# Kernel optimization log

Measured on AMD Instinct MI355X. Metric: run time of the kernel, lower is better.

## Reference

```python
import jax, jax.numpy as jnp
import numpy as np

# Dims: B=batch, T=attention source length, V=vector_size, A=attention_length (A==V forced by broadcast).
# TF Conv2D(kernel=(1,V), padding=SAME) on a [B,T,1,C] input has spatial width 1, so only the
# kernel column at pad_before=(V-1)//2 touches real data -> equivalent to a per-timestep matmul.
# We therefore materialize just that effective column (Wk_enc: [V,A], Kc_cov: [A] for the
# 1-channel coverage conv). Math is identical to the original layer.

def setup_inputs() -> dict:
    key = jax.random.key(0)
    ks = jax.random.split(key, 8)
    B, T, V = 32, 8192, 128
    A = V
    return {
        "encoder_state": jax.random.normal(ks[0], (B, T, V), jnp.float32),
        "decoder_state": jax.random.normal(ks[1], (B, V), jnp.float32),
        "input_mask": jnp.ones((B, T), jnp.float32),
        "coverage": jax.random.uniform(ks[2], (B, T, 1, 1), jnp.float32),
        "Wk_enc": jax.random.normal(ks[3], (V, A), jnp.float32) * 0.05,  # effective encoder conv column
        "b_enc": jnp.zeros((A,), jnp.float32),
        "W_dec": jax.random.normal(ks[4], (V, A), jnp.float32) * 0.05,  # Dense(vector_size)
        "b_dec": jnp.zeros((A,), jnp.float32),
        "Kc_cov": jax.random.normal(ks[5], (A,), jnp.float32) * 0.05,   # effective coverage conv column (1 in-channel)
        "b_cov": jnp.zeros((A,), jnp.float32),
        "v": jax.random.normal(ks[6], (A,), jnp.float32),
    }


def reference(encoder_state, decoder_state, input_mask, coverage,
              Wk_enc, b_enc, W_dec, b_dec, Kc_cov, b_cov, v):
    # encoder conv features: [B,T,A]
    enc_feat = jnp.einsum('btv,va->bta', encoder_state, Wk_enc) + b_enc
    # decoder dense features: [B,A]
    dec_feat = decoder_state @ W_dec + b_dec
    # coverage conv features: [B,T,A] (coverage has 1 channel, width 1)
    cov = coverage[:, :, 0, 0]                       # [B,T]
    cov_feat = cov[:, :, None] * Kc_cov + b_cov       # [B,T,A]
    # additive score: e[b,t] = sum_a v[a] * tanh(...)
    e = jnp.einsum('bta,a->bt',
                   jnp.tanh(enc_feat + dec_feat[:, None, :] + cov_feat), v)
    # masked softmax with renormalization
    attn = jax.nn.softmax(e, axis=-1) * input_mask
    attn = attn / jnp.sum(attn, axis=-1, keepdims=True)
    # coverage accumulation
    coverage_out = coverage + attn[:, :, None, None]
    # context vector: [B,V]
    context = jnp.einsum('bt,btv->bv', attn, encoder_state)
    return context, attn, coverage_out
```

## Files before the change

### kernel.cpp

```cpp
#include <hip/hip_runtime.h>
#include <hip/hip_bf16.h>
#include <math.h>

typedef __bf16 bf16x8 __attribute__((ext_vector_type(8)));
typedef float  f32x4  __attribute__((ext_vector_type(4)));

#define B_ 32
#define T_ 8192

__device__ __forceinline__ float tanh_fast(float x) {
  float ex = __expf(2.0f * x);
  return 1.0f - 2.0f / (ex + 1.0f);
}

__global__ __launch_bounds__(256) void setup_kernel(
    const float* __restrict__ dec, const float* __restrict__ b_enc,
    const float* __restrict__ W_dec, const float* __restrict__ b_dec,
    const float* __restrict__ b_cov, const float* __restrict__ Wk,
    float* __restrict__ addbuf, __bf16* __restrict__ wfrag)
{
  const int blk = blockIdx.x, tid = threadIdx.x;
  if (blk < 16) {
    const int idx = blk * 256 + tid;
    const int b = idx >> 7, a = idx & 127;
    float acc = b_dec[a] + b_enc[a] + b_cov[a];
    for (int k = 0; k < 128; ++k)
      acc += dec[b * 128 + k] * W_dec[k * 128 + a];
    addbuf[idx] = acc;
  } else {
    const int f = (blk - 16) * 256 + tid;
    const int l = f & 63;
    const int rest = f >> 6;
    const int ks = rest & 3, ct = rest >> 2;
    for (int j = 0; j < 8; ++j) {
      const int k = ks * 32 + (l >> 4) * 8 + j;
      const int a = ct * 16 + (l & 15);
      wfrag[f * 8 + j] = (__bf16)Wk[k * 128 + a];
    }
  }
}

__global__ __launch_bounds__(256, 4) void feat_ctx_kernel(
    const float* __restrict__ enc, const float* __restrict__ cov,
    const float* __restrict__ mask,
    const __bf16* __restrict__ wfrag_g, const float* __restrict__ addbuf,
    const float* __restrict__ Kc, const float* __restrict__ vvec,
    float* __restrict__ p_out, float* __restrict__ pctx,
    float* __restrict__ mblk, float* __restrict__ sblk)
{
  __shared__ __align__(16) float smem[8192];
  const int tid  = threadIdx.x;
  const int lane = tid & 63;
  const int w    = tid >> 6;
  const int lr   = lane & 15;
  const int lg   = lane >> 4;
  const long rowbase = (long)blockIdx.x * 128 + w * 32;
  const int b = (int)(rowbase >> 13);

  {
    const float4* src = (const float4*)wfrag_g;
    float4* dst = (float4*)smem;
#pragma unroll
    for (int i = 0; i < 8; ++i) dst[tid + i * 256] = src[tid + i * 256];
  }

  bf16x8 afrag[2][4];
#pragma unroll
  for (int rt = 0; rt < 2; ++rt) {
    const float* rp = enc + (rowbase + rt * 16 + lr) * 128;
#pragma unroll
    for (int ks = 0; ks < 4; ++ks) {
      const float4 f0 = *(const float4*)(rp + ks * 32 + lg * 8);
      const float4 f1 = *(const float4*)(rp + ks * 32 + lg * 8 + 4);
      bf16x8 t;
      t[0]=(__bf16)f0.x; t[1]=(__bf16)f0.y; t[2]=(__bf16)f0.z; t[3]=(__bf16)f0.w;
      t[4]=(__bf16)f1.x; t[5]=(__bf16)f1.y; t[6]=(__bf16)f1.z; t[7]=(__bf16)f1.w;
      afrag[rt][ks] = t;
    }
  }

  float addc[8], kcc[8], vc[8];
#pragma unroll
  for (int ct = 0; ct < 8; ++ct) {
    const int col = ct * 16 + lr;
    addc[ct] = addbuf[b * 128 + col];
    kcc[ct]  = Kc[col];
    vc[ct]   = vvec[col];
  }
  float cv8[2][4];
#pragma unroll
  for (int rt = 0; rt < 2; ++rt)
#pragma unroll
    for (int q = 0; q < 4; ++q)
      cv8[rt][q] = cov[rowbase + rt * 16 + lg * 4 + q];

  __syncthreads();

  float pacc[2][4];
#pragma unroll
  for (int rt = 0; rt < 2; ++rt)
#pragma unroll
    for (int q = 0; q < 4; ++q) pacc[rt][q] = 0.f;

  const bf16x8* wf = (const bf16x8*)smem;
#pragma unroll
  for (int ct = 0; ct < 8; ++ct) {
    bf16x8 bfr[4];
#pragma unroll
    for (int ks = 0; ks < 4; ++ks) bfr[ks] = wf[(ct * 4 + ks) * 64 + lane];
    f32x4 a0 = {0.f, 0.f, 0.f, 0.f};
    f32x4 a1 = {0.f, 0.f, 0.f, 0.f};
#pragma unroll
    for (int ks = 0; ks < 4; ++ks) {
      a0 = __builtin_amdgcn_mfma_f32_16x16x32_bf16(afrag[0][ks], bfr[ks], a0, 0, 0, 0);
      a1 = __builtin_amdgcn_mfma_f32_16x16x32_bf16(afrag[1][ks], bfr[ks], a1, 0, 0, 0);
    }
#pragma unroll
    for (int q = 0; q < 4; ++q) {
      const float x0 = a0[q] + addc[ct] + cv8[0][q] * kcc[ct];
      const float x1 = a1[q] + addc[ct] + cv8[1][q] * kcc[ct];
      pacc[0][q] += tanh_fast(x0) * vc[ct];
      pacc[1][q] += tanh_fast(x1) * vc[ct];
    }
  }

  float e8[2][4];
#pragma unroll
  for (int rt = 0; rt < 2; ++rt)
#pragma unroll
    for (int q = 0; q < 4; ++q) {
      float p = pacc[rt][q];
      p += __shfl_xor(p, 1); p += __shfl_xor(p, 2);
      p += __shfl_xor(p, 4); p += __shfl_xor(p, 8);
      e8[rt][q] = p;
    }

  float wm = e8[0][0];
#pragma unroll
  for (int rt = 0; rt < 2; ++rt)
#pragma unroll
    for (int q = 0; q < 4; ++q) wm = fmaxf(wm, e8[rt][q]);
  wm = fmaxf(wm, __shfl_xor(wm, 16));
  wm = fmaxf(wm, __shfl_xor(wm, 32));

  __syncthreads();
  float* red = smem;
  if (lane == 0) red[w] = wm;
  __syncthreads();
  const float m_loc = fmaxf(fmaxf(red[0], red[1]), fmaxf(red[2], red[3]));

  float p8[2][4];
  float ps = 0.f;
#pragma unroll
  for (int rt = 0; rt < 2; ++rt)
#pragma unroll
    for (int q = 0; q < 4; ++q) {
      const float mk = mask[rowbase + rt * 16 + lg * 4 + q];
      const float pv = __expf(e8[rt][q] - m_loc) * mk;
      p8[rt][q] = pv; ps += pv;
    }
#pragma unroll
  for (int off = 32; off > 0; off >>= 1) ps += __shfl_xor(ps, off);
  if (lane == 0) red[4 + w] = ps;
  __syncthreads();
  if (tid == 0) {
    sblk[blockIdx.x] = (red[4] + red[5] + red[6] + red[7]) * (1.0f / 16.0f);
    mblk[blockIdx.x] = m_loc;
  }

  float prow[2];
#pragma unroll
  for (int rt = 0; rt < 2; ++rt) {
    const int r3 = lr & 3;
    float sel = p8[rt][0];
    sel = (r3 == 1) ? p8[rt][1] : sel;
    sel = (r3 == 2) ? p8[rt][2] : sel;
    sel = (r3 == 3) ? p8[rt][3] : sel;
    prow[rt] = __shfl(sel, ((lr >> 2) << 4) | lr);
  }
  if (lg < 2) p_out[rowbase + lg * 16 + lr] = (lg == 0) ? prow[0] : prow[1];

  float ctxp[32];
#pragma unroll
  for (int c = 0; c < 32; ++c) ctxp[c] = 0.f;
#pragma unroll
  for (int rt = 0; rt < 2; ++rt) {
    const float pr = prow[rt];
#pragma unroll
    for (int ks = 0; ks < 4; ++ks)
#pragma unroll
      for (int j = 0; j < 8; ++j)
        ctxp[ks * 8 + j] += pr * (float)afrag[rt][ks][j];
  }
#pragma unroll
  for (int m = 1; m <= 8; m <<= 1)
#pragma unroll
    for (int c = 0; c < 32; ++c) ctxp[c] += __shfl_xor(ctxp[c], m);

  float* ctx_lds = smem + 8;
  if (lr == 0) {
#pragma unroll
    for (int ks = 0; ks < 4; ++ks)
#pragma unroll
      for (int j = 0; j < 8; ++j)
        ctx_lds[w * 128 + ks * 32 + lg * 8 + j] = ctxp[ks * 8 + j];
  }
  __syncthreads();
  if (tid < 128) {
    const float s = ctx_lds[tid] + ctx_lds[128 + tid] +
                    ctx_lds[256 + tid] + ctx_lds[384 + tid];
    pctx[(long)blockIdx.x * 128 + tid] = s;
  }
}

__global__ __launch_bounds__(128) void reduce_kernel(
    const float* __restrict__ mblk, const float* __restrict__ sblk,
    const float* __restrict__ pctx, float* __restrict__ alpha,
    float* __restrict__ ctx)
{
  const int b = blockIdx.x, tid = threadIdx.x;
  __shared__ float al[64];
  if (tid < 64) {
    const float mi = mblk[b * 64 + tid];
    const float si = sblk[b * 64 + tid];
    float m = mi;
#pragma unroll
    for (int off = 32; off > 0; off >>= 1) m = fmaxf(m, __shfl_xor(m, off));
    const float a = __expf(mi - m);
    float z = si * a;
#pragma unroll
    for (int off = 32; off > 0; off >>= 1) z += __shfl_xor(z, off);
    const float ai = a / z;
    al[tid] = ai;
    alpha[b * 64 + tid] = ai;
  }
  __syncthreads();
  float acc = 0.f;
#pragma unroll 8
  for (int i = 0; i < 64; ++i)
    acc += pctx[(long)(b * 64 + i) * 128 + tid] * al[i];
  ctx[b * 128 + tid] = acc;
}

__global__ __launch_bounds__(256) void finish_kernel(
    const float* __restrict__ p_buf, const float* __restrict__ alpha,
    const float* __restrict__ cov, float* __restrict__ attn,
    float* __restrict__ covout)
{
  const long idx = (long)blockIdx.x * 256 + threadIdx.x;
  const float a = p_buf[idx] * alpha[idx >> 7];
  attn[idx] = a;
  covout[idx] = cov[idx] + a;
}

extern "C" void kernel_launch(void* const* d_in, const int* in_sizes, int n_in,
                              void* d_out, int out_size, void* d_ws, size_t ws_size,
                              hipStream_t stream) {
  const float* enc   = (const float*)d_in[0];
  const float* dec   = (const float*)d_in[1];
  const float* mask  = (const float*)d_in[2];
  const float* cov   = (const float*)d_in[3];
  const float* Wk    = (const float*)d_in[4];
  const float* b_enc = (const float*)d_in[5];
  const float* W_dec = (const float*)d_in[6];
  const float* b_dec = (const float*)d_in[7];
  const float* Kc    = (const float*)d_in[8];
  const float* b_cov = (const float*)d_in[9];
  const float* vvec  = (const float*)d_in[10];

  float* out    = (float*)d_out;
  float* ctx    = out;
  float* attn   = out + B_ * 128;
  float* covout = attn + B_ * T_;

  char* ws = (char*)d_ws;
  __bf16* wfrag  = (__bf16*)ws;
  float*  addbuf = (float*)(ws + 32768);
  float*  p_buf  = (float*)(ws + 49152);
  float*  pctx   = (float*)(ws + 49152 + 1048576);
  float*  mblk   = (float*)(ws + 49152 + 2097152);
  float*  sblk   = (float*)(ws + 49152 + 2105344);
  float*  alpha  = (float*)(ws + 49152 + 2113536);

  setup_kernel   <<<24,   256, 0, stream>>>(dec, b_enc, W_dec, b_dec, b_cov, Wk,
                                            addbuf, wfrag);
  feat_ctx_kernel<<<2048, 256, 0, stream>>>(enc, cov, mask, wfrag, addbuf, Kc, vvec,
                                            p_buf, pctx, mblk, sblk);
  reduce_kernel  <<<32,   128, 0, stream>>>(mblk, sblk, pctx, alpha, ctx);
  finish_kernel  <<<1024, 256, 0, stream>>>(p_buf, alpha, cov, attn, covout);
}
```

Before: 57.06 us.

## Use transpose-style butterfly reductions and parallelize context reduce across more threads

Replaces the redundant xor-shuffle reductions of scores and context partials with recursive-halving butterflies, where each lane keeps half the values at every step. This cuts the shuffle count, especially for the 32-wide context vector. It also vectorizes the coverage load, drops one block barrier by moving the sblk/mblk writes to the end, and splits the per-batch reduce kernel over 1024 threads with an LDS combine. The risk is in the lane-to-row index mapping, which is more intricate and easy to get wrong.

```diff
diff --git a/kernel.cpp b/kernel.cpp
--- a/kernel.cpp
+++ b/kernel.cpp
@@ -87,12 +87,9 @@
     kcc[ct]  = Kc[col];
     vc[ct]   = vvec[col];
   }
-  float cv8[2][4];
-#pragma unroll
-  for (int rt = 0; rt < 2; ++rt)
-#pragma unroll
-    for (int q = 0; q < 4; ++q)
-      cv8[rt][q] = cov[rowbase + rt * 16 + lg * 4 + q];
+  const float4 cvA = *(const float4*)(cov + rowbase + lg * 4);
+  const float4 cvB = *(const float4*)(cov + rowbase + 16 + lg * 4);
+  float cv8[2][4] = {{cvA.x, cvA.y, cvA.z, cvA.w}, {cvB.x, cvB.y, cvB.z, cvB.w}};
 
   __syncthreads();
 
@@ -124,22 +121,34 @@
     }
   }
 
-  float e8[2][4];
-#pragma unroll
-  for (int rt = 0; rt < 2; ++rt)
-#pragma unroll
-    for (int q = 0; q < 4; ++q) {
-      float p = pacc[rt][q];
-      p += __shfl_xor(p, 1); p += __shfl_xor(p, 2);
-      p += __shfl_xor(p, 4); p += __shfl_xor(p, 8);
-      e8[rt][q] = p;
-    }
-
-  float wm = e8[0][0];
-#pragma unroll
-  for (int rt = 0; rt < 2; ++rt)
-#pragma unroll
-    for (int q = 0; q < 4; ++q) wm = fmaxf(wm, e8[rt][q]);
+  const bool b0 = (lr & 1), b1 = ((lr >> 1) & 1), b2 = ((lr >> 2) & 1);
+  float e4[4];
+#pragma unroll
+  for (int m = 0; m < 4; ++m) {
+    const float keep = b0 ? pacc[1][m] : pacc[0][m];
+    const float send = b0 ? pacc[0][m] : pacc[1][m];
+    e4[m] = keep + __shfl_xor(send, 1);
+  }
+  float e2[2];
+#pragma unroll
+  for (int m = 0; m < 2; ++m) {
+    const float keep = b1 ? e4[2 + m] : e4[m];
+    const float send = b1 ? e4[m] : e4[2 + m];
+    e2[m] = keep + __shfl_xor(send, 2);
+  }
+  float eo;
+  {
+    const float keep = b2 ? e2[1] : e2[0];
+    const float send = b2 ? e2[0] : e2[1];
+    eo = keep + __shfl_xor(send, 4);
+  }
+  eo += __shfl_xor(eo, 8);
+  const int row_own = (lr & 1) * 16 + lg * 4 + ((lr >> 1) & 1) * 2 + ((lr >> 2) & 1);
+
+  float wm = eo;
+  wm = fmaxf(wm, __shfl_xor(wm, 1));
+  wm = fmaxf(wm, __shfl_xor(wm, 2));
+  wm = fmaxf(wm, __shfl_xor(wm, 4));
   wm = fmaxf(wm, __shfl_xor(wm, 16));
   wm = fmaxf(wm, __shfl_xor(wm, 32));
 
@@ -149,34 +158,21 @@
   __syncthreads();
   const float m_loc = fmaxf(fmaxf(red[0], red[1]), fmaxf(red[2], red[3]));
 
-  float p8[2][4];
-  float ps = 0.f;
-#pragma unroll
-  for (int rt = 0; rt < 2; ++rt)
-#pragma unroll
-    for (int q = 0; q < 4; ++q) {
-      const float mk = mask[rowbase + rt * 16 + lg * 4 + q];
-      const float pv = __expf(e8[rt][q] - m_loc) * mk;
-      p8[rt][q] = pv; ps += pv;
-    }
-#pragma unroll
-  for (int off = 32; off > 0; off >>= 1) ps += __shfl_xor(ps, off);
+  const float p_own = __expf(eo - m_loc) * mask[rowbase + row_own];
+  float ps = p_own;
+  ps += __shfl_xor(ps, 1);
+  ps += __shfl_xor(ps, 2);
+  ps += __shfl_xor(ps, 4);
+  ps += __shfl_xor(ps, 16);
+  ps += __shfl_xor(ps, 32);
   if (lane == 0) red[4 + w] = ps;
-  __syncthreads();
-  if (tid == 0) {
-    sblk[blockIdx.x] = (red[4] + red[5] + red[6] + red[7]) * (1.0f / 16.0f);
-    mblk[blockIdx.x] = m_loc;
-  }
 
   float prow[2];
 #pragma unroll
   for (int rt = 0; rt < 2; ++rt) {
-    const int r3 = lr & 3;
-    float sel = p8[rt][0];
-    sel = (r3 == 1) ? p8[rt][1] : sel;
-    sel = (r3 == 2) ? p8[rt][2] : sel;
-    sel = (r3 == 3) ? p8[rt][3] : sel;
-    prow[rt] = __shfl(sel, ((lr >> 2) << 4) | lr);
+    const int q = lr & 3;
+    const int src = rt + ((q >> 1) << 1) + ((q & 1) << 2) + ((lr >> 2) << 4);
+    prow[rt] = __shfl(p_own, src);
   }
   if (lg < 2) p_out[rowbase + lg * 16 + lr] = (lg == 0) ? prow[0] : prow[1];
 
@@ -192,18 +188,42 @@
       for (int j = 0; j < 8; ++j)
         ctxp[ks * 8 + j] += pr * (float)afrag[rt][ks][j];
   }
-#pragma unroll
-  for (int m = 1; m <= 8; m <<= 1)
-#pragma unroll
-    for (int c = 0; c < 32; ++c) ctxp[c] += __shfl_xor(ctxp[c], m);
-
-  float* ctx_lds = smem + 8;
-  if (lr == 0) {
-#pragma unroll
-    for (int ks = 0; ks < 4; ++ks)
-#pragma unroll
-      for (int j = 0; j < 8; ++j)
-        ctx_lds[w * 128 + ks * 32 + lg * 8 + j] = ctxp[ks * 8 + j];
+
+  const bool b3 = ((lr >> 3) & 1);
+  float v16[16];
+#pragma unroll
+  for (int m = 0; m < 16; ++m) {
+    const float keep = b0 ? ctxp[2 * m + 1] : ctxp[2 * m];
+    const float send = b0 ? ctxp[2 * m] : ctxp[2 * m + 1];
+    v16[m] = keep + __shfl_xor(send, 1);
+  }
+  float v8[8];
+#pragma unroll
+  for (int m = 0; m < 8; ++m) {
+    const float keep = b1 ? v16[2 * m + 1] : v16[2 * m];
+    const float send = b1 ? v16[2 * m] : v16[2 * m + 1];
+    v8[m] = keep + __shfl_xor(send, 2);
+  }
+  float v4[4];
+#pragma unroll
+  for (int m = 0; m < 4; ++m) {
+    const float keep = b2 ? v8[2 * m + 1] : v8[2 * m];
+    const float send = b2 ? v8[2 * m] : v8[2 * m + 1];
+    v4[m] = keep + __shfl_xor(send, 4);
+  }
+  float v2[2];
+#pragma unroll
+  for (int m = 0; m < 2; ++m) {
+    const float keep = b3 ? v4[2 * m + 1] : v4[2 * m];
+    const float send = b3 ? v4[2 * m] : v4[2 * m + 1];
+    v2[m] = keep + __shfl_xor(send, 8);
+  }
+  float* ctx_lds = smem + 16;
+#pragma unroll
+  for (int m = 0; m < 2; ++m) {
+    const int c = 16 * m + lr;
+    const int v = (c >> 3) * 32 + lg * 8 + (c & 7);
+    ctx_lds[w * 128 + v] = v2[m];
   }
   __syncthreads();
   if (tid < 128) {
@@ -211,15 +231,20 @@
                     ctx_lds[256 + tid] + ctx_lds[384 + tid];
     pctx[(long)blockIdx.x * 128 + tid] = s;
   }
-}
-
-__global__ __launch_bounds__(128) void reduce_kernel(
+  if (tid == 0) {
+    sblk[blockIdx.x] = red[4] + red[5] + red[6] + red[7];
+    mblk[blockIdx.x] = m_loc;
+  }
+}
+
+__global__ __launch_bounds__(1024) void reduce_kernel(
     const float* __restrict__ mblk, const float* __restrict__ sblk,
     const float* __restrict__ pctx, float* __restrict__ alpha,
     float* __restrict__ ctx)
 {
   const int b = blockIdx.x, tid = threadIdx.x;
   __shared__ float al[64];
+  __shared__ float part[8][128];
   if (tid < 64) {
     const float mi = mblk[b * 64 + tid];
     const float si = sblk[b * 64 + tid];
@@ -235,11 +260,21 @@
     alpha[b * 64 + tid] = ai;
   }
   __syncthreads();
+  const int v = tid & 127, ch = tid >> 7;
   float acc = 0.f;
-#pragma unroll 8
-  for (int i = 0; i < 64; ++i)
-    acc += pctx[(long)(b * 64 + i) * 128 + tid] * al[i];
-  ctx[b * 128 + tid] = acc;
+#pragma unroll
+  for (int k = 0; k < 8; ++k) {
+    const int i = ch * 8 + k;
+    acc += pctx[(long)(b * 64 + i) * 128 + v] * al[i];
+  }
+  part[ch][v] = acc;
+  __syncthreads();
+  if (tid < 128) {
+    float s = 0.f;
+#pragma unroll
+    for (int c = 0; c < 8; ++c) s += part[c][tid];
+    ctx[b * 128 + tid] = s;
+  }
 }
 
 __global__ __launch_bounds__(256) void finish_kernel(
@@ -286,6 +321,6 @@
                                             addbuf, wfrag);
   feat_ctx_kernel<<<2048, 256, 0, stream>>>(enc, cov, mask, wfrag, addbuf, Kc, vvec,
                                             p_buf, pctx, mblk, sblk);
-  reduce_kernel  <<<32,   128, 0, stream>>>(mblk, sblk, pctx, alpha, ctx);
+  reduce_kernel  <<<32,  1024, 0, stream>>>(mblk, sblk, pctx, alpha, ctx);
   finish_kernel  <<<1024, 256, 0, stream>>>(p_buf, alpha, cov, attn, covout);
 }
```

After: 72.78 us. +27.5%, slower.

## Split context computation into a second fp32 pass over encoder state

Applied to the files above, without the earlier changes.

The feature kernel no longer computes partial context vectors. It now computes softmax statistics per wavefront instead of per block, which drops the block-level LDS reductions and barriers. A new alpha kernel turns the 256 per-chunk max/sum pairs into rescale factors. A fused ctx_attn kernel then rescales the probabilities, writes attn and coverage, and recomputes the context by re-reading the full fp32 encoder tensor, accumulating with atomicAdd. This aims to cut register pressure and synchronisation in the main kernel, but it reads the 128 MB encoder tensor a second time. Context is now computed in full fp32 rather than from bf16-converted values.

```diff
diff --git a/kernel.cpp b/kernel.cpp
--- a/kernel.cpp
+++ b/kernel.cpp
@@ -40,13 +40,13 @@
   }
 }
 
-__global__ __launch_bounds__(256, 4) void feat_ctx_kernel(
+__global__ __launch_bounds__(256, 4) void feat_kernel(
     const float* __restrict__ enc, const float* __restrict__ cov,
     const float* __restrict__ mask,
     const __bf16* __restrict__ wfrag_g, const float* __restrict__ addbuf,
     const float* __restrict__ Kc, const float* __restrict__ vvec,
-    float* __restrict__ p_out, float* __restrict__ pctx,
-    float* __restrict__ mblk, float* __restrict__ sblk)
+    float* __restrict__ p_out, float* __restrict__ mchunk,
+    float* __restrict__ schunk)
 {
   __shared__ __align__(16) float smem[8192];
   const int tid  = threadIdx.x;
@@ -54,7 +54,8 @@
   const int w    = tid >> 6;
   const int lr   = lane & 15;
   const int lg   = lane >> 4;
-  const long rowbase = (long)blockIdx.x * 128 + w * 32;
+  const int chunk = blockIdx.x * 4 + w;
+  const long rowbase = (long)chunk * 32;
   const int b = (int)(rowbase >> 13);
 
   {
@@ -79,20 +80,9 @@
     }
   }
 
-  float addc[8], kcc[8], vc[8];
-#pragma unroll
-  for (int ct = 0; ct < 8; ++ct) {
-    const int col = ct * 16 + lr;
-    addc[ct] = addbuf[b * 128 + col];
-    kcc[ct]  = Kc[col];
-    vc[ct]   = vvec[col];
-  }
-  float cv8[2][4];
-#pragma unroll
-  for (int rt = 0; rt < 2; ++rt)
-#pragma unroll
-    for (int q = 0; q < 4; ++q)
-      cv8[rt][q] = cov[rowbase + rt * 16 + lg * 4 + q];
+  const float4 cvA = *(const float4*)(cov + rowbase + lg * 4);
+  const float4 cvB = *(const float4*)(cov + rowbase + 16 + lg * 4);
+  float cv8[2][4] = {{cvA.x, cvA.y, cvA.z, cvA.w}, {cvB.x, cvB.y, cvB.z, cvB.w}};
 
   __syncthreads();
 
@@ -108,6 +98,10 @@
     bf16x8 bfr[4];
 #pragma unroll
     for (int ks = 0; ks < 4; ++ks) bfr[ks] = wf[(ct * 4 + ks) * 64 + lane];
+    const int col = ct * 16 + lr;
+    const float addc = addbuf[b * 128 + col];
+    const float kcc  = Kc[col];
+    const float vc   = vvec[col];
     f32x4 a0 = {0.f, 0.f, 0.f, 0.f};
     f32x4 a1 = {0.f, 0.f, 0.f, 0.f};
 #pragma unroll
@@ -117,10 +111,10 @@
     }
 #pragma unroll
     for (int q = 0; q < 4; ++q) {
-      const float x0 = a0[q] + addc[ct] + cv8[0][q] * kcc[ct];
-      const float x1 = a1[q] + addc[ct] + cv8[1][q] * kcc[ct];
-      pacc[0][q] += tanh_fast(x0) * vc[ct];
-      pacc[1][q] += tanh_fast(x1) * vc[ct];
+      const float x0 = a0[q] + addc + cv8[0][q] * kcc;
+      const float x1 = a1[q] + addc + cv8[1][q] * kcc;
+      pacc[0][q] += tanh_fast(x0) * vc;
+      pacc[1][q] += tanh_fast(x1) * vc;
     }
   }
 
@@ -135,19 +129,13 @@
       e8[rt][q] = p;
     }
 
-  float wm = e8[0][0];
-#pragma unroll
-  for (int rt = 0; rt < 2; ++rt)
-#pragma unroll
-    for (int q = 0; q < 4; ++q) wm = fmaxf(wm, e8[rt][q]);
-  wm = fmaxf(wm, __shfl_xor(wm, 16));
-  wm = fmaxf(wm, __shfl_xor(wm, 32));
-
-  __syncthreads();
-  float* red = smem;
-  if (lane == 0) red[w] = wm;
-  __syncthreads();
-  const float m_loc = fmaxf(fmaxf(red[0], red[1]), fmaxf(red[2], red[3]));
+  float m_loc = e8[0][0];
+#pragma unroll
+  for (int rt = 0; rt < 2; ++rt)
+#pragma unroll
+    for (int q = 0; q < 4; ++q) m_loc = fmaxf(m_loc, e8[rt][q]);
+  m_loc = fmaxf(m_loc, __shfl_xor(m_loc, 16));
+  m_loc = fmaxf(m_loc, __shfl_xor(m_loc, 32));
 
   float p8[2][4];
   float ps = 0.f;
@@ -159,14 +147,9 @@
       const float pv = __expf(e8[rt][q] - m_loc) * mk;
       p8[rt][q] = pv; ps += pv;
     }
-#pragma unroll
-  for (int off = 32; off > 0; off >>= 1) ps += __shfl_xor(ps, off);
-  if (lane == 0) red[4 + w] = ps;
-  __syncthreads();
-  if (tid == 0) {
-    sblk[blockIdx.x] = (red[4] + red[5] + red[6] + red[7]) * (1.0f / 16.0f);
-    mblk[blockIdx.x] = m_loc;
-  }
+  ps += __shfl_xor(ps, 16);
+  ps += __shfl_xor(ps, 32);
+  if (lane == 0) { schunk[chunk] = ps; mchunk[chunk] = m_loc; }
 
   float prow[2];
 #pragma unroll
@@ -179,78 +162,71 @@
     prow[rt] = __shfl(sel, ((lr >> 2) << 4) | lr);
   }
   if (lg < 2) p_out[rowbase + lg * 16 + lr] = (lg == 0) ? prow[0] : prow[1];
-
-  float ctxp[32];
-#pragma unroll
-  for (int c = 0; c < 32; ++c) ctxp[c] = 0.f;
-#pragma unroll
-  for (int rt = 0; rt < 2; ++rt) {
-    const float pr = prow[rt];
-#pragma unroll
-    for (int ks = 0; ks < 4; ++ks)
-#pragma unroll
-      for (int j = 0; j < 8; ++j)
-        ctxp[ks * 8 + j] += pr * (float)afrag[rt][ks][j];
-  }
-#pragma unroll
-  for (int m = 1; m <= 8; m <<= 1)
-#pragma unroll
-    for (int c = 0; c < 32; ++c) ctxp[c] += __shfl_xor(ctxp[c], m);
-
-  float* ctx_lds = smem + 8;
-  if (lr == 0) {
-#pragma unroll
-    for (int ks = 0; ks < 4; ++ks)
-#pragma unroll
-      for (int j = 0; j < 8; ++j)
-        ctx_lds[w * 128 + ks * 32 + lg * 8 + j] = ctxp[ks * 8 + j];
-  }
-  __syncthreads();
+}
+
+__global__ __launch_bounds__(256) void alpha_kernel(
+    const float* __restrict__ mchunk, const float* __restrict__ schunk,
+    float* __restrict__ alpha, float* __restrict__ ctx)
+{
+  const int b = blockIdx.x, tid = threadIdx.x;
+  __shared__ float red[8];
+  const float mi = mchunk[b * 256 + tid];
+  const float si = schunk[b * 256 + tid];
+  float m = mi;
+#pragma unroll
+  for (int off = 32; off > 0; off >>= 1) m = fmaxf(m, __shfl_xor(m, off));
+  if ((tid & 63) == 0) red[tid >> 6] = m;
+  __syncthreads();
+  const float m_all = fmaxf(fmaxf(red[0], red[1]), fmaxf(red[2], red[3]));
+  const float a = __expf(mi - m_all);
+  float z = si * a;
+#pragma unroll
+  for (int off = 32; off > 0; off >>= 1) z += __shfl_xor(z, off);
+  if ((tid & 63) == 0) red[4 + (tid >> 6)] = z;
+  __syncthreads();
+  const float Z = red[4] + red[5] + red[6] + red[7];
+  alpha[b * 256 + tid] = a / Z;
+  if (tid < 128) ctx[b * 128 + tid] = 0.f;
+}
+
+__global__ __launch_bounds__(256) void ctx_attn_kernel(
+    const float* __restrict__ enc, const float* __restrict__ p_buf,
+    const float* __restrict__ alpha, const float* __restrict__ cov,
+    float* __restrict__ attn, float* __restrict__ covout,
+    float* __restrict__ ctx)
+{
+  const int b  = blockIdx.x >> 6;
+  const int sp = blockIdx.x & 63;
+  const int tid = threadIdx.x;
+  const long rowbase = (long)b * T_ + sp * 128;
+  __shared__ float av[128];
+  __shared__ float sd[4][128];
   if (tid < 128) {
-    const float s = ctx_lds[tid] + ctx_lds[128 + tid] +
-                    ctx_lds[256 + tid] + ctx_lds[384 + tid];
-    pctx[(long)blockIdx.x * 128 + tid] = s;
-  }
-}
-
-__global__ __launch_bounds__(128) void reduce_kernel(
-    const float* __restrict__ mblk, const float* __restrict__ sblk,
-    const float* __restrict__ pctx, float* __restrict__ alpha,
-    float* __restrict__ ctx)
-{
-  const int b = blockIdx.x, tid = threadIdx.x;
-  __shared__ float al[64];
-  if (tid < 64) {
-    const float mi = mblk[b * 64 + tid];
-    const float si = sblk[b * 64 + tid];
-    float m = mi;
-#pragma unroll
-    for (int off = 32; off > 0; off >>= 1) m = fmaxf(m, __shfl_xor(m, off));
-    const float a = __expf(mi - m);
-    float z = si * a;
-#pragma unroll
-    for (int off = 32; off > 0; off >>= 1) z += __shfl_xor(z, off);
-    const float ai = a / z;
-    al[tid] = ai;
-    alpha[b * 64 + tid] = ai;
-  }
-  __syncthreads();
-  float acc = 0.f;
+    const long r = rowbase + tid;
+    const float a = p_buf[r] * alpha[r >> 5];
+    attn[r] = a;
+    covout[r] = cov[r] + a;
+    av[tid] = a;
+  }
+  __syncthreads();
+  const int cp = tid & 63;
+  const int rg = tid >> 6;
+  const float* ep = enc + rowbase * 128 + cp * 2;
+  float2 acc = make_float2(0.f, 0.f);
 #pragma unroll 8
-  for (int i = 0; i < 64; ++i)
-    acc += pctx[(long)(b * 64 + i) * 128 + tid] * al[i];
-  ctx[b * 128 + tid] = acc;
-}
-
-__global__ __launch_bounds__(256) void finish_kernel(
-    const float* __restrict__ p_buf, const float* __restrict__ alpha,
-    const float* __restrict__ cov, float* __restrict__ attn,
-    float* __restrict__ covout)
-{
-  const long idx = (long)blockIdx.x * 256 + threadIdx.x;
-  const float a = p_buf[idx] * alpha[idx >> 7];
-  attn[idx] = a;
-  covout[idx] = cov[idx] + a;
+  for (int i = 0; i < 32; ++i) {
+    const int r = i * 4 + rg;
+    const float wgt = av[r];
+    const float2 ev = *(const float2*)(ep + (long)r * 128);
+    acc.x += wgt * ev.x;
+    acc.y += wgt * ev.y;
+  }
+  ((float2*)sd[rg])[cp] = acc;
+  __syncthreads();
+  if (tid < 128) {
+    const float s = sd[0][tid] + sd[1][tid] + sd[2][tid] + sd[3][tid];
+    atomicAdd(&ctx[b * 128 + tid], s);
+  }
 }
 
 extern "C" void kernel_launch(void* const* d_in, const int* in_sizes, int n_in,
@@ -277,15 +253,15 @@
   __bf16* wfrag  = (__bf16*)ws;
   float*  addbuf = (float*)(ws + 32768);
   float*  p_buf  = (float*)(ws + 49152);
-  float*  pctx   = (float*)(ws + 49152 + 1048576);
-  float*  mblk   = (float*)(ws + 49152 + 2097152);
-  float*  sblk   = (float*)(ws + 49152 + 2105344);
-  float*  alpha  = (float*)(ws + 49152 + 2113536);
+  float*  mchunk = (float*)(ws + 49152 + 1048576);
+  float*  schunk = (float*)(ws + 49152 + 1081344);
+  float*  alpha  = (float*)(ws + 49152 + 1114112);
 
   setup_kernel   <<<24,   256, 0, stream>>>(dec, b_enc, W_dec, b_dec, b_cov, Wk,
                                             addbuf, wfrag);
-  feat_ctx_kernel<<<2048, 256, 0, stream>>>(enc, cov, mask, wfrag, addbuf, Kc, vvec,
-                                            p_buf, pctx, mblk, sblk);
-  reduce_kernel  <<<32,   128, 0, stream>>>(mblk, sblk, pctx, alpha, ctx);
-  finish_kernel  <<<1024, 256, 0, stream>>>(p_buf, alpha, cov, attn, covout);
-}
+  feat_kernel    <<<2048, 256, 0, stream>>>(enc, cov, mask, wfrag, addbuf, Kc, vvec,
+                                            p_buf, mchunk, schunk);
+  alpha_kernel   <<<32,   256, 0, stream>>>(mchunk, schunk, alpha, ctx);
+  ctx_attn_kernel<<<2048, 256, 0, stream>>>(enc, p_buf, alpha, cov,
+                                            attn, covout, ctx);
+}
```

New measurement: 67.13 us. +17.6%, slower.

## Drop LDS weight staging, trim syncs, and parallelize the context reduction

Applied to the files above, without the earlier changes.

The main kernel no longer copies the 32KB bf16 weight fragments into shared memory. Each wave reads them straight from global memory through the cache, which frees LDS and removes a barrier, so more blocks can be resident. It also drops the launch-bounds occupancy hint, vectorizes the coverage loads, shortens the partial-sum reduction, and uses a hardware reciprocal in tanh. The reduce kernel now spreads the 64-block context sum over 1024 threads instead of 128, at the cost of repeated global or L1 reads of the weights in every block.

```diff
diff --git a/kernel.cpp b/kernel.cpp
--- a/kernel.cpp
+++ b/kernel.cpp
@@ -9,8 +9,8 @@
 #define T_ 8192
 
 __device__ __forceinline__ float tanh_fast(float x) {
-  float ex = __expf(2.0f * x);
-  return 1.0f - 2.0f / (ex + 1.0f);
+  const float ex = __expf(2.0f * x);
+  return 1.0f - 2.0f * __builtin_amdgcn_rcpf(ex + 1.0f);
 }
 
 __global__ __launch_bounds__(256) void setup_kernel(
@@ -40,7 +40,7 @@
   }
 }
 
-__global__ __launch_bounds__(256, 4) void feat_ctx_kernel(
+__global__ void feat_ctx_kernel(
     const float* __restrict__ enc, const float* __restrict__ cov,
     const float* __restrict__ mask,
     const __bf16* __restrict__ wfrag_g, const float* __restrict__ addbuf,
@@ -48,7 +48,8 @@
     float* __restrict__ p_out, float* __restrict__ pctx,
     float* __restrict__ mblk, float* __restrict__ sblk)
 {
-  __shared__ __align__(16) float smem[8192];
+  __shared__ float red[16];
+  __shared__ float ctx_lds[4][128];
   const int tid  = threadIdx.x;
   const int lane = tid & 63;
   const int w    = tid >> 6;
@@ -57,13 +58,6 @@
   const long rowbase = (long)blockIdx.x * 128 + w * 32;
   const int b = (int)(rowbase >> 13);
 
-  {
-    const float4* src = (const float4*)wfrag_g;
-    float4* dst = (float4*)smem;
-#pragma unroll
-    for (int i = 0; i < 8; ++i) dst[tid + i * 256] = src[tid + i * 256];
-  }
-
   bf16x8 afrag[2][4];
 #pragma unroll
   for (int rt = 0; rt < 2; ++rt) {
@@ -87,14 +81,9 @@
     kcc[ct]  = Kc[col];
     vc[ct]   = vvec[col];
   }
-  float cv8[2][4];
-#pragma unroll
-  for (int rt = 0; rt < 2; ++rt)
-#pragma unroll
-    for (int q = 0; q < 4; ++q)
-      cv8[rt][q] = cov[rowbase + rt * 16 + lg * 4 + q];
-
-  __syncthreads();
+  const float4 cvA = *(const float4*)(cov + rowbase + lg * 4);
+  const float4 cvB = *(const float4*)(cov + rowbase + 16 + lg * 4);
+  float cv8[2][4] = {{cvA.x, cvA.y, cvA.z, cvA.w}, {cvB.x, cvB.y, cvB.z, cvB.w}};
 
   float pacc[2][4];
 #pragma unroll
@@ -102,12 +91,12 @@
 #pragma unroll
     for (int q = 0; q < 4; ++q) pacc[rt][q] = 0.f;
 
-  const bf16x8* wf = (const bf16x8*)smem;
+  const bf16x8* wf = (const bf16x8*)wfrag_g + lane;
 #pragma unroll
   for (int ct = 0; ct < 8; ++ct) {
     bf16x8 bfr[4];
 #pragma unroll
-    for (int ks = 0; ks < 4; ++ks) bfr[ks] = wf[(ct * 4 + ks) * 64 + lane];
+    for (int ks = 0; ks < 4; ++ks) bfr[ks] = wf[(ct * 4 + ks) * 64];
     f32x4 a0 = {0.f, 0.f, 0.f, 0.f};
     f32x4 a1 = {0.f, 0.f, 0.f, 0.f};
 #pragma unroll
@@ -143,8 +132,6 @@
   wm = fmaxf(wm, __shfl_xor(wm, 16));
   wm = fmaxf(wm, __shfl_xor(wm, 32));
 
-  __syncthreads();
-  float* red = smem;
   if (lane == 0) red[w] = wm;
   __syncthreads();
   const float m_loc = fmaxf(fmaxf(red[0], red[1]), fmaxf(red[2], red[3]));
@@ -159,14 +146,9 @@
       const float pv = __expf(e8[rt][q] - m_loc) * mk;
       p8[rt][q] = pv; ps += pv;
     }
-#pragma unroll
-  for (int off = 32; off > 0; off >>= 1) ps += __shfl_xor(ps, off);
-  if (lane == 0) red[4 + w] = ps;
-  __syncthreads();
-  if (tid == 0) {
-    sblk[blockIdx.x] = (red[4] + red[5] + red[6] + red[7]) * (1.0f / 16.0f);
-    mblk[blockIdx.x] = m_loc;
-  }
+  ps += __shfl_xor(ps, 16);
+  ps += __shfl_xor(ps, 32);
+  if (lane == 0) red[8 + w] = ps;
 
   float prow[2];
 #pragma unroll
@@ -197,29 +179,33 @@
 #pragma unroll
     for (int c = 0; c < 32; ++c) ctxp[c] += __shfl_xor(ctxp[c], m);
 
-  float* ctx_lds = smem + 8;
   if (lr == 0) {
 #pragma unroll
     for (int ks = 0; ks < 4; ++ks)
 #pragma unroll
       for (int j = 0; j < 8; ++j)
-        ctx_lds[w * 128 + ks * 32 + lg * 8 + j] = ctxp[ks * 8 + j];
+        ctx_lds[w][ks * 32 + lg * 8 + j] = ctxp[ks * 8 + j];
   }
   __syncthreads();
   if (tid < 128) {
-    const float s = ctx_lds[tid] + ctx_lds[128 + tid] +
-                    ctx_lds[256 + tid] + ctx_lds[384 + tid];
+    const float s = ctx_lds[0][tid] + ctx_lds[1][tid] +
+                    ctx_lds[2][tid] + ctx_lds[3][tid];
     pctx[(long)blockIdx.x * 128 + tid] = s;
   }
-}
-
-__global__ __launch_bounds__(128) void reduce_kernel(
+  if (tid == 0) {
+    sblk[blockIdx.x] = red[8] + red[9] + red[10] + red[11];
+    mblk[blockIdx.x] = m_loc;
+  }
+}
+
+__global__ __launch_bounds__(1024) void reduce_kernel(
     const float* __restrict__ mblk, const float* __restrict__ sblk,
     const float* __restrict__ pctx, float* __restrict__ alpha,
     float* __restrict__ ctx)
 {
   const int b = blockIdx.x, tid = threadIdx.x;
   __shared__ float al[64];
+  __shared__ float part[8][128];
   if (tid < 64) {
     const float mi = mblk[b * 64 + tid];
     const float si = sblk[b * 64 + tid];
@@ -235,11 +221,21 @@
     alpha[b * 64 + tid] = ai;
   }
   __syncthreads();
+  const int v = tid & 127, ch = tid >> 7;
   float acc = 0.f;
-#pragma unroll 8
-  for (int i = 0; i < 64; ++i)
-    acc += pctx[(long)(b * 64 + i) * 128 + tid] * al[i];
-  ctx[b * 128 + tid] = acc;
+#pragma unroll
+  for (int k = 0; k < 8; ++k) {
+    const int i = ch * 8 + k;
+    acc += pctx[(long)(b * 64 + i) * 128 + v] * al[i];
+  }
+  part[ch][v] = acc;
+  __syncthreads();
+  if (tid < 128) {
+    float s = 0.f;
+#pragma unroll
+    for (int c = 0; c < 8; ++c) s += part[c][tid];
+    ctx[b * 128 + tid] = s;
+  }
 }
 
 __global__ __launch_bounds__(256) void finish_kernel(
@@ -286,6 +282,6 @@
                                             addbuf, wfrag);
   feat_ctx_kernel<<<2048, 256, 0, stream>>>(enc, cov, mask, wfrag, addbuf, Kc, vvec,
                                             p_buf, pctx, mblk, sblk);
-  reduce_kernel  <<<32,   128, 0, stream>>>(mblk, sblk, pctx, alpha, ctx);
+  reduce_kernel  <<<32,  1024, 0, stream>>>(mblk, sblk, pctx, alpha, ctx);
   finish_kernel  <<<1024, 256, 0, stream>>>(p_buf, alpha, cov, attn, covout);
 }
```

New measurement: 82.69 us. 44.9% more time.
